# Optimization experiments

Hardware: AMD Instinct MI355X
Metric: run time of the kernel (lower is better)

## Reference

```python
import jax, jax.numpy as jnp
import numpy as np

B, S, H = 2, 1024, 1024        # batch, seq, hidden_size
E, I = 16, 512                 # n_routed_experts, moe_intermediate_size
TOP_K = 2                      # num_experts_per_tok
N_SHARED = 2                   # n_shared_experts -> shared intermediate = I * N_SHARED
SCALE = 1.0                    # routed_scaling_factor
IS = I * N_SHARED


def setup_inputs() -> dict:
    key = jax.random.key(0)
    ks = jax.random.split(key, 8)
    sd = 0.02
    return {
        "hidden_states": jax.random.normal(ks[0], (B, S, H), jnp.float32),
        "gate_w": jax.random.normal(ks[1], (E, H), jnp.float32) * sd,   # router weight [E, H]
        "w_gate": jax.random.normal(ks[2], (E, H, I), jnp.float32) * sd,
        "w_up":   jax.random.normal(ks[3], (E, H, I), jnp.float32) * sd,
        "w_down": jax.random.normal(ks[4], (E, I, H), jnp.float32) * sd,
        "ws_gate": jax.random.normal(ks[5], (H, IS), jnp.float32) * sd,
        "ws_up":   jax.random.normal(ks[6], (H, IS), jnp.float32) * sd,
        "ws_down": jax.random.normal(ks[7], (IS, H), jnp.float32) * sd,
    }


def reference(hidden_states, gate_w, w_gate, w_up, w_down, ws_gate, ws_up, ws_down):
    b, s, h = hidden_states.shape
    x = hidden_states.reshape(-1, h)                      # [T, H]
    T = x.shape[0]

    # ---- gate (greedy top-k over softmax of router logits, fp32) ----
    logits = jnp.einsum('th,eh->te', x.astype(jnp.float32), gate_w.astype(jnp.float32))
    scores = jax.nn.softmax(logits, axis=-1)              # [T, E]
    topk_w, topk_idx = jax.lax.top_k(scores, TOP_K)       # [T, K]
    topk_w = topk_w * SCALE

    # combine weights as dense [T, E] (equivalent to argsort dispatch + scatter combine)
    combine = jnp.zeros((T, E), jnp.float32).at[
        jnp.arange(T)[:, None], topk_idx].add(topk_w)     # [T, E]

    # ---- routed experts: SwiGLU MLP per expert, weighted combine ----
    g = jnp.einsum('th,ehi->tei', x, w_gate)              # [T, E, I]
    u = jnp.einsum('th,ehi->tei', x, w_up)                # [T, E, I]
    act = jax.nn.silu(g) * u                              # [T, E, I]
    # fuse down-proj with combine weights to avoid a [T, E, H] intermediate
    routed = jnp.einsum('tei,eih,te->th', act, w_down, combine)  # [T, H]

    # ---- shared experts on the residual ----
    sg = jax.nn.silu(x @ ws_gate) * (x @ ws_up)           # [T, IS]
    shared = sg @ ws_down                                 # [T, H]

    return (routed + shared).reshape(b, s, h)
```

## Files before the change

kernel.cpp:

```cpp
#include <hip/hip_runtime.h>
#include <hip/hip_bf16.h>

#define T_TOK 2048
#define H_DIM 1024
#define NEXP  16
#define I_DIM 512
#define CAP   384
#define RSCALE 1.0f

typedef unsigned short u16;
typedef unsigned int   u32;
typedef __attribute__((ext_vector_type(4))) float  f32x4;
typedef __attribute__((ext_vector_type(8))) __bf16 bf16x8;
typedef __attribute__((ext_vector_type(8))) u16    u16x8;
typedef __attribute__((ext_vector_type(4))) u16    u16x4;

__device__ __forceinline__ u16 f2bf(float f) {
  u32 u = __builtin_bit_cast(u32, f);
  u32 r = u + 0x7fffu + ((u >> 16) & 1u);
  return (u16)(r >> 16);
}
__device__ __forceinline__ float bf2f(u16 h) {
  return __builtin_bit_cast(float, (u32)h << 16);
}
__device__ __forceinline__ void gload16(const void* g, void* l) {
  __builtin_amdgcn_global_load_lds((const __attribute__((address_space(1))) u32*)g,
                                   (__attribute__((address_space(3))) u32*)l, 16, 0, 0);
}

__device__ __forceinline__ void transpose_tile(const float* __restrict__ src, int srcN,
                                               int k0, int n0,
                                               u16* __restrict__ dst, int dstride, int drow0)
{
  __shared__ float t[64][65];
  int tid = threadIdx.x;
  int kl = tid >> 4, c4 = (tid & 15) * 4;
  #pragma unroll
  for (int p = 0; p < 4; ++p) {
    f32x4 v = *(const f32x4*)(src + (size_t)(k0 + p*16 + kl) * srcN + n0 + c4);
    #pragma unroll
    for (int j = 0; j < 4; ++j) t[p*16 + kl][c4 + j] = v[j];
  }
  __syncthreads();
  int nl = tid >> 3, kc = (tid & 7) * 8;
  #pragma unroll
  for (int p = 0; p < 2; ++p) {
    int n = p*32 + nl;
    u16x8 o;
    #pragma unroll
    for (int j = 0; j < 8; ++j) o[j] = f2bf(t[kc + j][n]);
    *(u16x8*)(dst + (size_t)(drow0 + n) * dstride + k0 + kc) = o;
  }
}

__global__ __launch_bounds__(256) void convert_kernel(
    const float* __restrict__ x,
    const float* __restrict__ w_gate, const float* __restrict__ w_up,
    const float* __restrict__ w_down,
    const float* __restrict__ wsg, const float* __restrict__ wsu,
    const float* __restrict__ wsd,
    u16* __restrict__ xb, u16* __restrict__ wgu_t, u16* __restrict__ wd_t,
    u16* __restrict__ wsgu_t, u16* __restrict__ wsd_t)
{
  int tile = blockIdx.x, tid = threadIdx.x;
  if (tile < 512) {
    #pragma unroll
    for (int p = 0; p < 4; ++p) {
      int fi = tile*1024 + p*256 + tid;
      f32x4 v = ((const f32x4*)x)[fi];
      u16x4 o;
      #pragma unroll
      for (int j = 0; j < 4; ++j) o[j] = f2bf(v[j]);
      ((u16x4*)xb)[fi] = o;
    }
  } else if (tile < 4608) {
    int t2 = tile - 512; int e = t2 >> 8; int r = t2 & 255;
    int mat = r >> 7; int q = r & 127; int kt = q >> 3, nt = q & 7;
    const float* src = (mat ? w_up : w_gate) + (size_t)e * H_DIM * I_DIM;
    transpose_tile(src, I_DIM, kt*64, nt*64,
                   wgu_t + (size_t)e * 1024 * 1024, 1024, mat*512 + nt*64);
  } else if (tile < 6656) {
    int t2 = tile - 4608; int e = t2 >> 7; int q = t2 & 127;
    int kt = q >> 4, nt = q & 15;
    transpose_tile(w_down + (size_t)e * I_DIM * H_DIM, H_DIM, kt*64, nt*64,
                   wd_t + (size_t)e * 1024 * 512, 512, nt*64);
  } else if (tile < 7168) {
    int t2 = tile - 6656; int mat = t2 >> 8; int q = t2 & 255;
    int kt = q >> 4, nt = q & 15;
    transpose_tile(mat ? wsu : wsg, 1024, kt*64, nt*64,
                   wsgu_t, 1024, mat*1024 + nt*64);
  } else {
    int t2 = tile - 7168; int kt = t2 >> 4, nt = t2 & 15;
    transpose_tile(wsd, H_DIM, kt*64, nt*64, wsd_t, 1024, nt*64);
  }
}

__global__ __launch_bounds__(256) void router_kernel(
    const float* __restrict__ x, const float* __restrict__ gw,
    int* __restrict__ perm_tok, int* __restrict__ slot_of,
    float* __restrict__ tok_w, int* __restrict__ counts)
{
  __shared__ f32x4 gws[4096];
  int tid = threadIdx.x;
  const f32x4* gw4 = (const f32x4*)gw;
  #pragma unroll
  for (int i = 0; i < 16; ++i) gws[i*256 + tid] = gw4[i*256 + tid];
  __syncthreads();

  int wv = tid >> 6, l = tid & 63;
  int t0 = blockIdx.x * 16 + wv * 4;

  f32x4 xv[4][4];
  #pragma unroll
  for (int tk = 0; tk < 4; ++tk) {
    const f32x4* xr = (const f32x4*)(x + (size_t)(t0 + tk) * H_DIM);
    #pragma unroll
    for (int j = 0; j < 4; ++j) xv[tk][j] = xr[j*64 + l];
  }

  float p[4][NEXP];
  #pragma unroll
  for (int tk = 0; tk < 4; ++tk)
    #pragma unroll
    for (int e = 0; e < NEXP; ++e) p[tk][e] = 0.f;

  #pragma unroll
  for (int j = 0; j < 4; ++j)
    #pragma unroll
    for (int e = 0; e < NEXP; ++e) {
      f32x4 g = gws[e*256 + j*64 + l];
      #pragma unroll
      for (int tk = 0; tk < 4; ++tk)
        p[tk][e] += xv[tk][j][0]*g[0] + xv[tk][j][1]*g[1]
                  + xv[tk][j][2]*g[2] + xv[tk][j][3]*g[3];
    }

  #pragma unroll
  for (int tk = 0; tk < 4; ++tk)
    #pragma unroll
    for (int e = 0; e < NEXP; ++e)
      #pragma unroll
      for (int off = 32; off; off >>= 1)
        p[tk][e] += __shfl_xor(p[tk][e], off);

  if (l < 4) {
    int tk = l;
    int t = t0 + tk;
    float m = p[tk][0];
    #pragma unroll
    for (int e = 1; e < NEXP; ++e) m = fmaxf(m, p[tk][e]);
    float q[NEXP]; float s = 0.f;
    #pragma unroll
    for (int e = 0; e < NEXP; ++e) { q[e] = expf(p[tk][e] - m); s += q[e]; }
    float inv = 1.f / s;
    int e1 = 0; float b1 = -1.f;
    #pragma unroll
    for (int e = 0; e < NEXP; ++e) if (q[e] > b1) { b1 = q[e]; e1 = e; }
    int e2 = -1; float b2 = -1.f;
    #pragma unroll
    for (int e = 0; e < NEXP; ++e) if (e != e1 && q[e] > b2) { b2 = q[e]; e2 = e; }

    tok_w[2*t]   = b1 * inv * RSCALE;
    tok_w[2*t+1] = b2 * inv * RSCALE;
    int p1 = atomicAdd(&counts[e1], 1);
    if (p1 < CAP) { perm_tok[e1*CAP + p1] = t; slot_of[2*t] = e1*CAP + p1; }
    else slot_of[2*t] = -1;
    int p2 = atomicAdd(&counts[e2], 1);
    if (p2 < CAP) { perm_tok[e2*CAP + p2] = t; slot_of[2*t+1] = e2*CAP + p2; }
    else slot_of[2*t+1] = -1;
  }
}

template<bool GU>
__global__ __launch_bounds__(256, 2) void gemm_fused_kernel(
    const u16* __restrict__ A_sh, const u16* __restrict__ A_rt,
    const u16* __restrict__ B_sh, const u16* __restrict__ B_rt,
    u16* __restrict__ C_sh, u16* __restrict__ C_rt,
    float* __restrict__ O_sh, float* __restrict__ O_rt,
    const int* __restrict__ counts, const int* __restrict__ perm_tok)
{
  int b = blockIdx.x;
  bool routed = b < 384;

  int kdim, m0, m_end, n0, cstr;
  const u16 *A, *B;
  u16* C; float* O;
  bool gather = false;

  if (routed) {
    int e  = b / 24;
    int r  = b % 24;
    int my = r >> 3, nx = r & 7;
    int cnt = counts[e]; if (cnt > CAP) cnt = CAP;
    int m_start = e * CAP;
    m_end = m_start + cnt;
    m0 = m_start + my * 128;
    if (m0 >= m_end) return;
    n0 = nx * 128;
    if (GU) {
      kdim = 1024; A = A_rt; gather = true;
      B = B_rt + ((size_t)e << 20);
      C = C_rt; cstr = 1024; O = nullptr;
    } else {
      kdim = 512;  A = A_rt;
      B = B_rt + ((size_t)e << 19);
      C = nullptr; cstr = 0; O = O_rt;
    }
  } else {
    int s = b - 384;
    kdim = 1024;
    if (GU) {
      int my = s >> 4, nx = s & 15;
      m0 = my * 128; n0 = nx * 128; m_end = T_TOK;
      A = A_sh; B = B_sh; C = C_sh; cstr = 2048; O = nullptr;
    } else {
      int my = s >> 3, nx = s & 7;
      m0 = my * 128; n0 = nx * 128; m_end = T_TOK;
      A = A_sh; B = B_sh; C = nullptr; cstr = 0; O = O_sh;
    }
  }

  __shared__ __align__(16) u16 lds[2][2][8192];
  int tid = threadIdx.x;
  int wv = tid >> 6, l = tid & 63;
  int wm = wv >> 1, wn = wv & 1;
  int rl = tid >> 3;
  int c8 = (tid & 7) * 8;

  f32x4 acc[4][4];
  #pragma unroll
  for (int m = 0; m < 4; ++m)
    #pragma unroll
    for (int n = 0; n < 4; ++n) acc[m][n] = f32x4{0.f, 0.f, 0.f, 0.f};

  auto stage = [&](int buf, int kt) {
    int k0 = kt * 64;
    #pragma unroll
    for (int i = 0; i < 4; ++i) {
      int slot = m0 + i*32 + rl;
      int srow = slot < m_end ? slot : m_end - 1;
      int grow = gather ? perm_tok[srow] : srow;
      gload16(A + (size_t)grow * kdim + k0 + c8, &lds[buf][0][i*2048 + wv*512]);
    }
    #pragma unroll
    for (int i = 0; i < 4; ++i) {
      gload16(B + (size_t)(n0 + i*32 + rl) * kdim + k0 + c8, &lds[buf][1][i*2048 + wv*512]);
    }
  };

  stage(0, 0);
  __syncthreads();
  const int NK = kdim >> 6;
  for (int kt = 0; kt < NK; ++kt) {
    int buf = kt & 1;
    if (kt + 1 < NK) stage(buf ^ 1, kt + 1);
    const u16* At  = &lds[buf][0][0];
    const u16* Btl = &lds[buf][1][0];
    #pragma unroll
    for (int kk = 0; kk < 2; ++kk) {
      bf16x8 af[4], bv[4];
      int ko = kk*32 + (l >> 4) * 8;
      #pragma unroll
      for (int m = 0; m < 4; ++m)
        af[m] = *(const bf16x8*)(At + (wm*64 + m*16 + (l & 15)) * 64 + ko);
      #pragma unroll
      for (int n = 0; n < 4; ++n)
        bv[n] = *(const bf16x8*)(Btl + (wn*64 + n*16 + (l & 15)) * 64 + ko);
      #pragma unroll
      for (int m = 0; m < 4; ++m)
        #pragma unroll
        for (int n = 0; n < 4; ++n)
          acc[m][n] = __builtin_amdgcn_mfma_f32_16x16x32_bf16(af[m], bv[n], acc[m][n], 0, 0, 0);
    }
    __syncthreads();
  }

  #pragma unroll
  for (int m = 0; m < 4; ++m) {
    #pragma unroll
    for (int n = 0; n < 4; ++n) {
      int col = n0 + wn*64 + n*16 + (l & 15);
      #pragma unroll
      for (int r = 0; r < 4; ++r) {
        int slot = m0 + wm*64 + m*16 + (l >> 4)*4 + r;
        if (slot >= m_end) continue;
        float v = acc[m][n][r];
        if (GU) C[(size_t)slot * cstr + col] = f2bf(v);
        else    O[(size_t)slot * H_DIM + col] = v;
      }
    }
  }
}

__global__ __launch_bounds__(256) void silumul_kernel(
    const u16* __restrict__ gu_r, const u16* __restrict__ gu_s,
    u16* __restrict__ act_r, u16* __restrict__ act_s,
    const int* __restrict__ counts)
{
  int b = blockIdx.x;
  if (b < 1536) {
    int idx = b * 256 + threadIdx.x;
    int s = idx >> 6;
    int i8 = (idx & 63) * 8;
    int e = s / CAP, pos = s - e * CAP;
    if (pos >= counts[e]) return;
    u16x8 g = *(const u16x8*)(gu_r + (size_t)s*1024 + i8);
    u16x8 u = *(const u16x8*)(gu_r + (size_t)s*1024 + 512 + i8);
    u16x8 o;
    #pragma unroll
    for (int j = 0; j < 8; ++j) {
      float gf = bf2f(g[j]), uf = bf2f(u[j]);
      o[j] = f2bf(gf / (1.f + expf(-gf)) * uf);
    }
    *(u16x8*)(act_r + (size_t)s*I_DIM + i8) = o;
  } else {
    int idx = (b - 1536) * 256 + threadIdx.x;
    int s = idx >> 7;
    int i8 = (idx & 127) * 8;
    u16x8 g = *(const u16x8*)(gu_s + (size_t)s*2048 + i8);
    u16x8 u = *(const u16x8*)(gu_s + (size_t)s*2048 + 1024 + i8);
    u16x8 o;
    #pragma unroll
    for (int j = 0; j < 8; ++j) {
      float gf = bf2f(g[j]), uf = bf2f(u[j]);
      o[j] = f2bf(gf / (1.f + expf(-gf)) * uf);
    }
    *(u16x8*)(act_s + (size_t)s*1024 + i8) = o;
  }
}

__global__ __launch_bounds__(256) void combine_kernel(
    float* __restrict__ out, const float* __restrict__ down_r,
    const int* __restrict__ slot_of, const float* __restrict__ tok_w)
{
  int t = blockIdx.x, c = threadIdx.x;
  f32x4* orow = (f32x4*)(out + (size_t)t * H_DIM);
  f32x4 o = orow[c];
  int s0 = slot_of[2*t], s1 = slot_of[2*t+1];
  float w0 = tok_w[2*t], w1 = tok_w[2*t+1];
  if (s0 >= 0) {
    f32x4 v = ((const f32x4*)(down_r + (size_t)s0 * H_DIM))[c];
    o += v * w0;
  }
  if (s1 >= 0) {
    f32x4 v = ((const f32x4*)(down_r + (size_t)s1 * H_DIM))[c];
    o += v * w1;
  }
  orow[c] = o;
}

extern "C" void kernel_launch(void* const* d_in, const int* in_sizes, int n_in,
                              void* d_out, int out_size, void* d_ws, size_t ws_size,
                              hipStream_t stream)
{
  (void)in_sizes; (void)n_in; (void)out_size;
  const float* x       = (const float*)d_in[0];
  const float* gate_w  = (const float*)d_in[1];
  const float* w_gate  = (const float*)d_in[2];
  const float* w_up    = (const float*)d_in[3];
  const float* w_down  = (const float*)d_in[4];
  const float* wsg     = (const float*)d_in[5];
  const float* wsu     = (const float*)d_in[6];
  const float* wsd     = (const float*)d_in[7];
  float* out = (float*)d_out;

  char* base = (char*)d_ws;
  size_t off = 0;
  auto alloc = [&](size_t n) -> void* {
    void* r = base + off;
    off += (n + 255) & ~(size_t)255;
    return r;
  };
  u16* xb       = (u16*)alloc((size_t)T_TOK * H_DIM * 2);
  u16* wgu_t    = (u16*)alloc((size_t)NEXP * 1024 * 1024 * 2);
  u16* wd_t     = (u16*)alloc((size_t)NEXP * 1024 * 512 * 2);
  u16* wsgu_t   = (u16*)alloc((size_t)2048 * 1024 * 2);
  u16* wsd_t    = (u16*)alloc((size_t)1024 * 1024 * 2);
  u16* gu_r     = (u16*)alloc((size_t)NEXP * CAP * 1024 * 2);
  u16* gu_s     = (u16*)alloc((size_t)2048 * 2048 * 2);
  int*   counts   = (int*)alloc(64);
  int*   tok_w_i  = (int*)alloc((size_t)2 * T_TOK * 4);
  int*   slot_of  = (int*)alloc((size_t)2 * T_TOK * 4);
  int*   perm_tok = (int*)alloc((size_t)NEXP * CAP * 4);
  float* tok_w = (float*)tok_w_i;
  u16*   act_s  = xb;
  float* down_r = (float*)wgu_t;
  u16*   act_r  = (u16*)((char*)wgu_t + (24u<<20));
  if (off > ws_size) return;

  hipMemsetAsync(counts, 0, 64, stream);
  convert_kernel<<<7424, 256, 0, stream>>>(x, w_gate, w_up, w_down, wsg, wsu, wsd,
                                           xb, wgu_t, wd_t, wsgu_t, wsd_t);
  router_kernel<<<128, 256, 0, stream>>>(x, gate_w, perm_tok, slot_of, tok_w, counts);
  gemm_fused_kernel<true><<<640, 256, 0, stream>>>(
      xb, xb, wsgu_t, wgu_t, gu_s, gu_r, nullptr, nullptr, counts, perm_tok);
  silumul_kernel<<<2560, 256, 0, stream>>>(gu_r, gu_s, act_r, act_s, counts);
  gemm_fused_kernel<false><<<512, 256, 0, stream>>>(
      act_s, act_r, wsd_t, wd_t, nullptr, nullptr, out, down_r, counts, perm_tok);
  combine_kernel<<<T_TOK, 256, 0, stream>>>(out, down_r, slot_of, tok_w);
}
```

Baseline: 268.8 us.

## Interleave gate/up weight columns and fuse SiLU-mul into the gate-up GEMM epilogue

```diff
diff --git a/kernel.cpp b/kernel.cpp
--- a/kernel.cpp
+++ b/kernel.cpp
@@ -30,7 +30,8 @@
 
 __device__ __forceinline__ void transpose_tile(const float* __restrict__ src, int srcN,
                                                int k0, int n0,
-                                               u16* __restrict__ dst, int dstride, int drow0)
+                                               u16* __restrict__ dst, int dstride,
+                                               int drow0, int rmul)
 {
   __shared__ float t[64][65];
   int tid = threadIdx.x;
@@ -49,7 +50,7 @@
     u16x8 o;
     #pragma unroll
     for (int j = 0; j < 8; ++j) o[j] = f2bf(t[kc + j][n]);
-    *(u16x8*)(dst + (size_t)(drow0 + n) * dstride + k0 + kc) = o;
+    *(u16x8*)(dst + (size_t)(drow0 + n*rmul) * dstride + k0 + kc) = o;
   }
 }
 
@@ -78,20 +79,20 @@
     int mat = r >> 7; int q = r & 127; int kt = q >> 3, nt = q & 7;
     const float* src = (mat ? w_up : w_gate) + (size_t)e * H_DIM * I_DIM;
     transpose_tile(src, I_DIM, kt*64, nt*64,
-                   wgu_t + (size_t)e * 1024 * 1024, 1024, mat*512 + nt*64);
+                   wgu_t + (size_t)e * 1024 * 1024, 1024, nt*128 + mat, 2);
   } else if (tile < 6656) {
     int t2 = tile - 4608; int e = t2 >> 7; int q = t2 & 127;
     int kt = q >> 4, nt = q & 15;
     transpose_tile(w_down + (size_t)e * I_DIM * H_DIM, H_DIM, kt*64, nt*64,
-                   wd_t + (size_t)e * 1024 * 512, 512, nt*64);
+                   wd_t + (size_t)e * 1024 * 512, 512, nt*64, 1);
   } else if (tile < 7168) {
     int t2 = tile - 6656; int mat = t2 >> 8; int q = t2 & 255;
     int kt = q >> 4, nt = q & 15;
     transpose_tile(mat ? wsu : wsg, 1024, kt*64, nt*64,
-                   wsgu_t, 1024, mat*1024 + nt*64);
+                   wsgu_t, 1024, nt*128 + mat, 2);
   } else {
     int t2 = tile - 7168; int kt = t2 >> 4, nt = t2 & 15;
-    transpose_tile(wsd, H_DIM, kt*64, nt*64, wsd_t, 1024, nt*64);
+    transpose_tile(wsd, H_DIM, kt*64, nt*64, wsd_t, 1024, nt*64, 1);
   }
 }
 
@@ -200,7 +201,7 @@
     if (GU) {
       kdim = 1024; A = A_rt; gather = true;
       B = B_rt + ((size_t)e << 20);
-      C = C_rt; cstr = 1024; O = nullptr;
+      C = C_rt; cstr = 512; O = nullptr;
     } else {
       kdim = 512;  A = A_rt;
       B = B_rt + ((size_t)e << 19);
@@ -212,7 +213,7 @@
     if (GU) {
       int my = s >> 4, nx = s & 15;
       m0 = my * 128; n0 = nx * 128; m_end = T_TOK;
-      A = A_sh; B = B_sh; C = C_sh; cstr = 2048; O = nullptr;
+      A = A_sh; B = B_sh; C = C_sh; cstr = 1024; O = nullptr;
     } else {
       int my = s >> 3, nx = s & 7;
       m0 = my * 128; n0 = nx * 128; m_end = T_TOK;
@@ -283,49 +284,20 @@
       #pragma unroll
       for (int r = 0; r < 4; ++r) {
         int slot = m0 + wm*64 + m*16 + (l >> 4)*4 + r;
-        if (slot >= m_end) continue;
-        float v = acc[m][n][r];
-        if (GU) C[(size_t)slot * cstr + col] = f2bf(v);
-        else    O[(size_t)slot * H_DIM + col] = v;
+        if (GU) {
+          float own = acc[m][n][r];
+          float oth = __shfl_xor(own, 1);
+          float g = (l & 1) ? oth : own;
+          float u = (l & 1) ? own : oth;
+          float actv = g / (1.f + expf(-g)) * u;
+          if (!(l & 1) && slot < m_end)
+            C[(size_t)slot * cstr + (col >> 1)] = f2bf(actv);
+        } else {
+          if (slot < m_end)
+            O[(size_t)slot * H_DIM + col] = acc[m][n][r];
+        }
       }
     }
-  }
-}
-
-__global__ __launch_bounds__(256) void silumul_kernel(
-    const u16* __restrict__ gu_r, const u16* __restrict__ gu_s,
-    u16* __restrict__ act_r, u16* __restrict__ act_s,
-    const int* __restrict__ counts)
-{
-  int b = blockIdx.x;
-  if (b < 1536) {
-    int idx = b * 256 + threadIdx.x;
-    int s = idx >> 6;
-    int i8 = (idx & 63) * 8;
-    int e = s / CAP, pos = s - e * CAP;
-    if (pos >= counts[e]) return;
-    u16x8 g = *(const u16x8*)(gu_r + (size_t)s*1024 + i8);
-    u16x8 u = *(const u16x8*)(gu_r + (size_t)s*1024 + 512 + i8);
-    u16x8 o;
-    #pragma unroll
-    for (int j = 0; j < 8; ++j) {
-      float gf = bf2f(g[j]), uf = bf2f(u[j]);
-      o[j] = f2bf(gf / (1.f + expf(-gf)) * uf);
-    }
-    *(u16x8*)(act_r + (size_t)s*I_DIM + i8) = o;
-  } else {
-    int idx = (b - 1536) * 256 + threadIdx.x;
-    int s = idx >> 7;
-    int i8 = (idx & 127) * 8;
-    u16x8 g = *(const u16x8*)(gu_s + (size_t)s*2048 + i8);
-    u16x8 u = *(const u16x8*)(gu_s + (size_t)s*2048 + 1024 + i8);
-    u16x8 o;
-    #pragma unroll
-    for (int j = 0; j < 8; ++j) {
-      float gf = bf2f(g[j]), uf = bf2f(u[j]);
-      o[j] = f2bf(gf / (1.f + expf(-gf)) * uf);
-    }
-    *(u16x8*)(act_s + (size_t)s*1024 + i8) = o;
   }
 }
 
@@ -376,16 +348,14 @@
   u16* wd_t     = (u16*)alloc((size_t)NEXP * 1024 * 512 * 2);
   u16* wsgu_t   = (u16*)alloc((size_t)2048 * 1024 * 2);
   u16* wsd_t    = (u16*)alloc((size_t)1024 * 1024 * 2);
-  u16* gu_r     = (u16*)alloc((size_t)NEXP * CAP * 1024 * 2);
-  u16* gu_s     = (u16*)alloc((size_t)2048 * 2048 * 2);
+  u16* act_r    = (u16*)alloc((size_t)NEXP * CAP * I_DIM * 2);
+  u16* act_s    = (u16*)alloc((size_t)T_TOK * 1024 * 2);
   int*   counts   = (int*)alloc(64);
   int*   tok_w_i  = (int*)alloc((size_t)2 * T_TOK * 4);
   int*   slot_of  = (int*)alloc((size_t)2 * T_TOK * 4);
   int*   perm_tok = (int*)alloc((size_t)NEXP * CAP * 4);
   float* tok_w = (float*)tok_w_i;
-  u16*   act_s  = xb;
   float* down_r = (float*)wgu_t;
-  u16*   act_r  = (u16*)((char*)wgu_t + (24u<<20));
   if (off > ws_size) return;
 
   hipMemsetAsync(counts, 0, 64, stream);
@@ -393,8 +363,7 @@
                                            xb, wgu_t, wd_t, wsgu_t, wsd_t);
   router_kernel<<<128, 256, 0, stream>>>(x, gate_w, perm_tok, slot_of, tok_w, counts);
   gemm_fused_kernel<true><<<640, 256, 0, stream>>>(
-      xb, xb, wsgu_t, wgu_t, gu_s, gu_r, nullptr, nullptr, counts, perm_tok);
-  silumul_kernel<<<2560, 256, 0, stream>>>(gu_r, gu_s, act_r, act_s, counts);
+      xb, xb, wsgu_t, wgu_t, act_s, act_r, nullptr, nullptr, counts, perm_tok);
   gemm_fused_kernel<false><<<512, 256, 0, stream>>>(
       act_s, act_r, wsd_t, wd_t, nullptr, nullptr, out, down_r, counts, perm_tok);
   combine_kernel<<<T_TOK, 256, 0, stream>>>(out, down_r, slot_of, tok_w);
```

New measurement: 271.3 us. About the same (+0.9%).
